# Kernel tuning notes

Hardware: AMD Instinct MI355X
Metric: run time of the kernel (lower is better)

The kernel has to match this reference:

```python
import jax, jax.numpy as jnp
import numpy as np

N_HEAD = 12

def setup_inputs() -> dict:
    key = jax.random.key(0)
    k1, k2, k3 = jax.random.split(key, 3)
    B, T, C = 8, 1024, 768
    x = jax.random.normal(k1, (B, T, C), dtype=jnp.float32)
    # torch nn.Linear weight layout: [out_features, in_features]
    W_attn = jax.random.normal(k2, (3 * C, C), dtype=jnp.float32) * 0.02
    b_attn = jax.random.normal(k3, (3 * C,), dtype=jnp.float32) * 0.02
    return {"x": x, "W_attn": W_attn, "b_attn": b_attn}

def reference(x, W_attn, b_attn):
    B, T, C = x.shape
    H = N_HEAD
    hs = C // H
    scale = 1.0 / jnp.sqrt(jnp.asarray(hs, x.dtype))
    # fused qkv projection: x @ W^T + b  -> [B, T, 3C]
    qkv = jnp.einsum('btc,oc->bto', x, W_attn) + b_attn
    qkv = qkv.reshape(B, T, 3, H, hs).transpose(2, 0, 3, 1, 4)  # [3, B, H, T, hs]
    q, k, v = qkv[0], qkv[1], qkv[2]
    scores = jnp.einsum('bhqd,bhkd->bhqk', q, k) * scale  # [B, H, T, T]
    causal = jnp.tril(jnp.ones((T, T), dtype=bool))
    # masked_fill(-inf) followed by ReLU == zero out masked positions after ReLU
    att = jnp.where(causal, jax.nn.relu(scores), jnp.zeros((), scores.dtype))
    y = jnp.einsum('bhqk,bhkd->bhqd', att, v)  # [B, H, T, hs]
    return y.transpose(0, 2, 1, 3).reshape(B, T, C)
```

## Files before the change

### kernel.cpp

```cpp
#include <hip/hip_runtime.h>
#include <hip/hip_bf16.h>
#include <stdint.h>

#define T_ 1024
#define C_ 768
#define H_ 12
#define HS 64

typedef __attribute__((ext_vector_type(8))) short bf16x8;
typedef __attribute__((ext_vector_type(4))) float f32x4;

#define GLOAD16(g, l) __builtin_amdgcn_global_load_lds( \
    (const __attribute__((address_space(1))) uint32_t*)(g), \
    (__attribute__((address_space(3))) uint32_t*)(l), 16, 0, 0)

__device__ __forceinline__ ushort f2b(float f) {
  uint32_t u = __builtin_bit_cast(uint32_t, f);
  u = (u + 0x7fffu + ((u >> 16) & 1u)) >> 16;
  return (ushort)u;
}

__global__ __launch_bounds__(256) void cvt_bf16(
    const float* __restrict__ x, const float* __restrict__ wt,
    ushort* __restrict__ xb, ushort* __restrict__ wb) {
  const int NX4 = 8192 * 768 / 4;
  const int NW4 = 2304 * 768 / 4;
  int i = blockIdx.x * 256 + threadIdx.x;
  int stride = gridDim.x * 256;
  for (int idx = i; idx < NX4; idx += stride) {
    float4 f = ((const float4*)x)[idx];
    ushort4 o;
    o.x = f2b(f.x); o.y = f2b(f.y); o.z = f2b(f.z); o.w = f2b(f.w);
    ((ushort4*)xb)[idx] = o;
  }
  for (int idx = i; idx < NW4; idx += stride) {
    float4 f = ((const float4*)wt)[idx];
    ushort4 o;
    o.x = f2b(f.x); o.y = f2b(f.y); o.z = f2b(f.z); o.w = f2b(f.w);
    ((ushort4*)wb)[idx] = o;
  }
}

__global__ __launch_bounds__(256) void qkv_gemm(
    const ushort* __restrict__ xb, const ushort* __restrict__ wb,
    const float* __restrict__ bias,
    ushort* __restrict__ qo, ushort* __restrict__ ko, ushort* __restrict__ vo) {
  __shared__ __align__(16) ushort As[128 * 64];
  __shared__ __align__(16) ushort Bs[128 * 64];
  const int tid = threadIdx.x, lane = tid & 63, w = tid >> 6;
  const int g = lane >> 4, l15 = lane & 15;
  const int m0 = blockIdx.y * 128, n0 = blockIdx.x * 128;
  const int wr = w >> 1, wc = w & 1;
  f32x4 acc[4][4] = {};

  for (int kk = 0; kk < 12; ++kk) {
    const int k0 = kk * 64;
    #pragma unroll
    for (int c = 0; c < 4; ++c) {
      int p = (w * 4 + c) * 64 + lane;
      int row = p >> 3, s = p & 7;
      int sc = (s ^ (row & 7)) * 8;
      GLOAD16(xb + (size_t)(m0 + row) * 768 + k0 + sc, (char*)As + (w * 4 + c) * 1024);
      GLOAD16(wb + (size_t)(n0 + row) * 768 + k0 + sc, (char*)Bs + (w * 4 + c) * 1024);
    }
    __syncthreads();
    #pragma unroll
    for (int kd = 0; kd < 2; ++kd) {
      bf16x8 af[4], bf[4];
      #pragma unroll
      for (int mi = 0; mi < 4; ++mi) {
        int row = wr * 64 + mi * 16 + l15;
        af[mi] = *(const bf16x8*)((const char*)As + row * 128 + (((kd * 4 + g) ^ (row & 7)) << 4));
      }
      #pragma unroll
      for (int ni = 0; ni < 4; ++ni) {
        int row = wc * 64 + ni * 16 + l15;
        bf[ni] = *(const bf16x8*)((const char*)Bs + row * 128 + (((kd * 4 + g) ^ (row & 7)) << 4));
      }
      #pragma unroll
      for (int mi = 0; mi < 4; ++mi)
        #pragma unroll
        for (int ni = 0; ni < 4; ++ni)
          acc[mi][ni] = __builtin_amdgcn_mfma_f32_16x16x32_bf16(af[mi], bf[ni], acc[mi][ni], 0, 0, 0);
    }
    __syncthreads();
  }

  const int which = n0 / 768;
  ushort* outp = (which == 0) ? qo : (which == 1) ? ko : vo;
  #pragma unroll
  for (int ni = 0; ni < 4; ++ni) {
    int n = n0 + wc * 64 + ni * 16 + l15;
    float bn = bias[n];
    int nin = n - which * 768;
    int h = nin >> 6, d = nin & 63;
    #pragma unroll
    for (int mi = 0; mi < 4; ++mi) {
      #pragma unroll
      for (int r = 0; r < 4; ++r) {
        int m = m0 + wr * 64 + mi * 16 + g * 4 + r;
        float val = acc[mi][ni][r] + bn;
        outp[((size_t)((m >> 10) * H_ + h) * T_ + (m & (T_ - 1))) * HS + d] = f2b(val);
      }
    }
  }
}

__global__ __launch_bounds__(256) void transpose_v(
    const ushort* __restrict__ v, ushort* __restrict__ vT) {
  __shared__ __align__(16) ushort Ts[64 * 64];
  const int tid = threadIdx.x;
  const int bh = blockIdx.x, tt = blockIdx.y;
  const size_t base = (size_t)bh * (T_ * HS);
  #pragma unroll
  for (int c = 0; c < 2; ++c) {
    int p = c * 256 + tid;
    int row = p >> 3, s = p & 7;
    *(uint4*)((char*)Ts + row * 128 + ((s ^ (row & 7)) << 4)) =
        *(const uint4*)(v + base + (size_t)(tt * 64 + row) * HS + s * 8);
  }
  __syncthreads();
  #pragma unroll
  for (int c = 0; c < 2; ++c) {
    int p = c * 256 + tid;
    int d = p >> 3, s = p & 7, t0 = s * 8;
    ushort tmp[8];
    #pragma unroll
    for (int j = 0; j < 8; ++j) {
      int t = t0 + j;
      tmp[j] = *(const ushort*)((const char*)Ts + t * 128 + ((2 * d) ^ ((t & 7) << 4)));
    }
    uint4 pk;
    pk.x = (uint)tmp[0] | ((uint)tmp[1] << 16);
    pk.y = (uint)tmp[2] | ((uint)tmp[3] << 16);
    pk.z = (uint)tmp[4] | ((uint)tmp[5] << 16);
    pk.w = (uint)tmp[6] | ((uint)tmp[7] << 16);
    *(uint4*)(vT + base + (size_t)d * T_ + tt * 64 + t0) = pk;
  }
}

__global__ __launch_bounds__(256) void attn_relu(
    const ushort* __restrict__ q, const ushort* __restrict__ k,
    const ushort* __restrict__ vT, float* __restrict__ out) {
  __shared__ __align__(16) ushort Qs[64 * 64];
  __shared__ __align__(16) ushort Ks[64 * 64];
  __shared__ __align__(16) ushort VTs[64 * 64];
  __shared__ __align__(16) ushort Ps[64 * 64];
  const int tid = threadIdx.x, lane = tid & 63, w = tid >> 6;
  const int g = lane >> 4, l15 = lane & 15;
  const int bh = blockIdx.x, qt = blockIdx.y;
  const int q0 = qt * 64;
  const size_t base = (size_t)bh * (T_ * HS);

  #pragma unroll
  for (int c = 0; c < 2; ++c) {
    int p = (w * 2 + c) * 64 + lane;
    int row = p >> 3, s = p & 7;
    int sc = (s ^ (row & 7)) * 8;
    GLOAD16(q + base + (size_t)(q0 + row) * HS + sc, (char*)Qs + (w * 2 + c) * 1024);
  }

  f32x4 yacc[4] = {};
  const int qrow = w * 16 + l15;
  const int nkt = qt + 1;

  for (int kt = 0; kt < nkt; ++kt) {
    #pragma unroll
    for (int c = 0; c < 2; ++c) {
      int p = (w * 2 + c) * 64 + lane;
      int row = p >> 3, s = p & 7;
      int sc = (s ^ (row & 7)) * 8;
      GLOAD16(k + base + (size_t)(kt * 64 + row) * HS + sc, (char*)Ks + (w * 2 + c) * 1024);
      GLOAD16(vT + base + (size_t)row * T_ + kt * 64 + sc, (char*)VTs + (w * 2 + c) * 1024);
    }
    __syncthreads();

    f32x4 sacc[4] = {};
    #pragma unroll
    for (int kd = 0; kd < 2; ++kd) {
      bf16x8 qf = *(const bf16x8*)((const char*)Qs + qrow * 128 + (((kd * 4 + g) ^ (qrow & 7)) << 4));
      #pragma unroll
      for (int nt = 0; nt < 4; ++nt) {
        int krow = nt * 16 + l15;
        bf16x8 kf = *(const bf16x8*)((const char*)Ks + krow * 128 + (((kd * 4 + g) ^ (krow & 7)) << 4));
        sacc[nt] = __builtin_amdgcn_mfma_f32_16x16x32_bf16(qf, kf, sacc[nt], 0, 0, 0);
      }
    }

    #pragma unroll
    for (int nt = 0; nt < 4; ++nt) {
      int kj = kt * 64 + nt * 16 + l15;
      #pragma unroll
      for (int r = 0; r < 4; ++r) {
        int i = w * 16 + g * 4 + r;
        float sv = sacc[nt][r] * 0.125f;
        float pv = (kj <= q0 + i) ? fmaxf(sv, 0.0f) : 0.0f;
        *(ushort*)((char*)Ps + i * 128 + (((nt * 16 + l15) * 2) ^ ((i & 7) << 4))) = f2b(pv);
      }
    }

    bf16x8 pf[2], vf[2][4];
    #pragma unroll
    for (int kj2 = 0; kj2 < 2; ++kj2) {
      pf[kj2] = *(const bf16x8*)((const char*)Ps + qrow * 128 + (((kj2 * 4 + g) ^ (qrow & 7)) << 4));
      #pragma unroll
      for (int nt = 0; nt < 4; ++nt) {
        int vrow = nt * 16 + l15;
        vf[kj2][nt] = *(const bf16x8*)((const char*)VTs + vrow * 128 + (((kj2 * 4 + g) ^ (vrow & 7)) << 4));
      }
    }
    #pragma unroll
    for (int kj2 = 0; kj2 < 2; ++kj2)
      #pragma unroll
      for (int nt = 0; nt < 4; ++nt)
        yacc[nt] = __builtin_amdgcn_mfma_f32_16x16x32_bf16(pf[kj2], vf[kj2][nt], yacc[nt], 0, 0, 0);

    __syncthreads();
  }

  const int bb = bh / H_, hh = bh % H_;
  #pragma unroll
  for (int nt = 0; nt < 4; ++nt) {
    #pragma unroll
    for (int r = 0; r < 4; ++r) {
      int t = q0 + w * 16 + g * 4 + r;
      int col = hh * HS + nt * 16 + l15;
      out[(size_t)(bb * T_ + t) * C_ + col] = yacc[nt][r];
    }
  }
}

extern "C" void kernel_launch(void* const* d_in, const int* in_sizes, int n_in,
                              void* d_out, int out_size, void* d_ws, size_t ws_size,
                              hipStream_t stream) {
  const float* x    = (const float*)d_in[0];
  const float* W    = (const float*)d_in[1];
  const float* bias = (const float*)d_in[2];
  float* out = (float*)d_out;

  char* ws = (char*)d_ws;
  ushort* xb = (ushort*)ws;
  ushort* wb = (ushort*)(ws + 12582912);
  ushort* qb = (ushort*)(ws + 16121856);
  ushort* kb = (ushort*)(ws + 28704768);
  ushort* vb = (ushort*)(ws + 41287680);
  ushort* vT = xb;

  cvt_bf16<<<2048, 256, 0, stream>>>(x, W, xb, wb);
  qkv_gemm<<<dim3(18, 64), 256, 0, stream>>>(xb, wb, bias, qb, kb, vb);
  transpose_v<<<dim3(96, 16), 256, 0, stream>>>(vb, vT);
  attn_relu<<<dim3(96, 16), 256, 0, stream>>>(qb, kb, vT, out);
}
```

Measured before the change: 174.5 us.

## Double-buffer GEMM and attention loads, fuse V transpose into QKV epilogue

The QKV GEMM now uses a double-buffered LDS pipeline over 32-wide K slices, prefetching the next slice while the current one is multiplied. Its V-output blocks write V transposed through shared memory, so the separate transpose kernel and one launch go away. The attention kernel double-buffers K/V tiles, keeps Q in registers, and reverses the query-tile order so the longest causal tiles are scheduled first. The costs are more LDS per block, which may lower occupancy, and a more complex epilogue.

```diff
diff --git a/kernel.cpp b/kernel.cpp
--- a/kernel.cpp
+++ b/kernel.cpp
@@ -44,146 +44,166 @@
 __global__ __launch_bounds__(256) void qkv_gemm(
     const ushort* __restrict__ xb, const ushort* __restrict__ wb,
     const float* __restrict__ bias,
-    ushort* __restrict__ qo, ushort* __restrict__ ko, ushort* __restrict__ vo) {
-  __shared__ __align__(16) ushort As[128 * 64];
-  __shared__ __align__(16) ushort Bs[128 * 64];
+    ushort* __restrict__ qo, ushort* __restrict__ ko, ushort* __restrict__ vT) {
+  __shared__ __align__(16) ushort smem[16384];
   const int tid = threadIdx.x, lane = tid & 63, w = tid >> 6;
   const int g = lane >> 4, l15 = lane & 15;
   const int m0 = blockIdx.y * 128, n0 = blockIdx.x * 128;
   const int wr = w >> 1, wc = w & 1;
   f32x4 acc[4][4] = {};
 
-  for (int kk = 0; kk < 12; ++kk) {
-    const int k0 = kk * 64;
-    #pragma unroll
-    for (int c = 0; c < 4; ++c) {
-      int p = (w * 4 + c) * 64 + lane;
-      int row = p >> 3, s = p & 7;
-      int sc = (s ^ (row & 7)) * 8;
-      GLOAD16(xb + (size_t)(m0 + row) * 768 + k0 + sc, (char*)As + (w * 4 + c) * 1024);
-      GLOAD16(wb + (size_t)(n0 + row) * 768 + k0 + sc, (char*)Bs + (w * 4 + c) * 1024);
-    }
+  const ushort* srcA[2];
+  const ushort* srcB[2];
+  int dstoff[2];
+  #pragma unroll
+  for (int c = 0; c < 2; ++c) {
+    int p = (c * 4 + w) * 64 + lane;
+    int row = p >> 2, s = p & 3;
+    int sc = (s ^ ((row >> 1) & 3)) * 8;
+    srcA[c] = xb + (size_t)(m0 + row) * 768 + sc;
+    srcB[c] = wb + (size_t)(n0 + row) * 768 + sc;
+    dstoff[c] = (c * 4 + w) * 1024;
+  }
+
+#define STAGE_G(buf, k0) do { \
+    char* bb_ = (char*)smem + (buf) * 16384; \
+    _Pragma("unroll") \
+    for (int c_ = 0; c_ < 2; ++c_) { \
+      GLOAD16(srcA[c_] + (k0), bb_ + dstoff[c_]); \
+      GLOAD16(srcB[c_] + (k0), bb_ + 8192 + dstoff[c_]); \
+    } \
+  } while (0)
+
+  int cur = 0;
+  STAGE_G(0, 0);
+  __syncthreads();
+  #pragma unroll 2
+  for (int kk = 0; kk < 24; ++kk) {
+    if (kk < 23) STAGE_G(cur ^ 1, (kk + 1) * 32);
+    const char* Ab = (const char*)smem + cur * 16384;
+    const char* Bb = Ab + 8192;
+    bf16x8 af[4], bfr[4];
+    #pragma unroll
+    for (int mi = 0; mi < 4; ++mi) {
+      int r = wr * 64 + mi * 16 + l15;
+      af[mi] = *(const bf16x8*)(Ab + r * 64 + ((g ^ ((r >> 1) & 3)) << 4));
+    }
+    #pragma unroll
+    for (int ni = 0; ni < 4; ++ni) {
+      int r = wc * 64 + ni * 16 + l15;
+      bfr[ni] = *(const bf16x8*)(Bb + r * 64 + ((g ^ ((r >> 1) & 3)) << 4));
+    }
+    #pragma unroll
+    for (int mi = 0; mi < 4; ++mi)
+      #pragma unroll
+      for (int ni = 0; ni < 4; ++ni)
+        acc[mi][ni] = __builtin_amdgcn_mfma_f32_16x16x32_bf16(af[mi], bfr[ni], acc[mi][ni], 0, 0, 0);
     __syncthreads();
-    #pragma unroll
-    for (int kd = 0; kd < 2; ++kd) {
-      bf16x8 af[4], bf[4];
+    cur ^= 1;
+  }
+
+  const int which = n0 / 768;
+  if (which < 2) {
+    ushort* outp = (which == 0) ? qo : ko;
+    #pragma unroll
+    for (int ni = 0; ni < 4; ++ni) {
+      int n = n0 + wc * 64 + ni * 16 + l15;
+      float bn = bias[n];
+      int nin = n - which * 768;
+      int h = nin >> 6, d = nin & 63;
       #pragma unroll
       for (int mi = 0; mi < 4; ++mi) {
-        int row = wr * 64 + mi * 16 + l15;
-        af[mi] = *(const bf16x8*)((const char*)As + row * 128 + (((kd * 4 + g) ^ (row & 7)) << 4));
-      }
-      #pragma unroll
-      for (int ni = 0; ni < 4; ++ni) {
-        int row = wc * 64 + ni * 16 + l15;
-        bf[ni] = *(const bf16x8*)((const char*)Bs + row * 128 + (((kd * 4 + g) ^ (row & 7)) << 4));
-      }
-      #pragma unroll
-      for (int mi = 0; mi < 4; ++mi)
         #pragma unroll
-        for (int ni = 0; ni < 4; ++ni)
-          acc[mi][ni] = __builtin_amdgcn_mfma_f32_16x16x32_bf16(af[mi], bf[ni], acc[mi][ni], 0, 0, 0);
+        for (int r = 0; r < 4; ++r) {
+          int m = m0 + wr * 64 + mi * 16 + g * 4 + r;
+          float val = acc[mi][ni][r] + bn;
+          outp[((size_t)((m >> 10) * H_ + h) * T_ + (m & (T_ - 1))) * HS + d] = f2b(val);
+        }
+      }
+    }
+  } else {
+    #pragma unroll
+    for (int ni = 0; ni < 4; ++ni) {
+      int n = n0 + wc * 64 + ni * 16 + l15;
+      float bn = bias[n];
+      int dl = wc * 64 + ni * 16 + l15;
+      #pragma unroll
+      for (int mi = 0; mi < 4; ++mi) {
+        #pragma unroll
+        for (int r = 0; r < 4; ++r) {
+          int tl = wr * 64 + mi * 16 + g * 4 + r;
+          *(ushort*)((char*)smem + dl * 256 + ((tl * 2) ^ ((dl & 7) << 4))) =
+              f2b(acc[mi][ni][r] + bn);
+        }
+      }
     }
     __syncthreads();
-  }
-
-  const int which = n0 / 768;
-  ushort* outp = (which == 0) ? qo : (which == 1) ? ko : vo;
-  #pragma unroll
-  for (int ni = 0; ni < 4; ++ni) {
-    int n = n0 + wc * 64 + ni * 16 + l15;
-    float bn = bias[n];
-    int nin = n - which * 768;
-    int h = nin >> 6, d = nin & 63;
-    #pragma unroll
-    for (int mi = 0; mi < 4; ++mi) {
-      #pragma unroll
-      for (int r = 0; r < 4; ++r) {
-        int m = m0 + wr * 64 + mi * 16 + g * 4 + r;
-        float val = acc[mi][ni][r] + bn;
-        outp[((size_t)((m >> 10) * H_ + h) * T_ + (m & (T_ - 1))) * HS + d] = f2b(val);
-      }
-    }
-  }
-}
-
-__global__ __launch_bounds__(256) void transpose_v(
-    const ushort* __restrict__ v, ushort* __restrict__ vT) {
-  __shared__ __align__(16) ushort Ts[64 * 64];
-  const int tid = threadIdx.x;
-  const int bh = blockIdx.x, tt = blockIdx.y;
-  const size_t base = (size_t)bh * (T_ * HS);
-  #pragma unroll
-  for (int c = 0; c < 2; ++c) {
-    int p = c * 256 + tid;
-    int row = p >> 3, s = p & 7;
-    *(uint4*)((char*)Ts + row * 128 + ((s ^ (row & 7)) << 4)) =
-        *(const uint4*)(v + base + (size_t)(tt * 64 + row) * HS + s * 8);
-  }
-  __syncthreads();
-  #pragma unroll
-  for (int c = 0; c < 2; ++c) {
-    int p = c * 256 + tid;
-    int d = p >> 3, s = p & 7, t0 = s * 8;
-    ushort tmp[8];
-    #pragma unroll
-    for (int j = 0; j < 8; ++j) {
-      int t = t0 + j;
-      tmp[j] = *(const ushort*)((const char*)Ts + t * 128 + ((2 * d) ^ ((t & 7) << 4)));
-    }
-    uint4 pk;
-    pk.x = (uint)tmp[0] | ((uint)tmp[1] << 16);
-    pk.y = (uint)tmp[2] | ((uint)tmp[3] << 16);
-    pk.z = (uint)tmp[4] | ((uint)tmp[5] << 16);
-    pk.w = (uint)tmp[6] | ((uint)tmp[7] << 16);
-    *(uint4*)(vT + base + (size_t)d * T_ + tt * 64 + t0) = pk;
+    const int b = m0 >> 10, t0base = m0 & 1023;
+    #pragma unroll
+    for (int c = 0; c < 8; ++c) {
+      int p = c * 256 + tid;
+      int dl = p >> 4, tch = p & 15;
+      uint4 val = *(const uint4*)((const char*)smem + dl * 256 + ((tch * 16) ^ ((dl & 7) << 4)));
+      int nin = n0 + dl - 1536;
+      int h = nin >> 6, dd = nin & 63;
+      *(uint4*)(vT + (((size_t)(b * H_ + h) * HS + dd) << 10) + t0base + tch * 8) = val;
+    }
   }
 }
 
 __global__ __launch_bounds__(256) void attn_relu(
     const ushort* __restrict__ q, const ushort* __restrict__ k,
     const ushort* __restrict__ vT, float* __restrict__ out) {
-  __shared__ __align__(16) ushort Qs[64 * 64];
-  __shared__ __align__(16) ushort Ks[64 * 64];
-  __shared__ __align__(16) ushort VTs[64 * 64];
-  __shared__ __align__(16) ushort Ps[64 * 64];
+  __shared__ __align__(16) ushort smem[20480];
   const int tid = threadIdx.x, lane = tid & 63, w = tid >> 6;
   const int g = lane >> 4, l15 = lane & 15;
-  const int bh = blockIdx.x, qt = blockIdx.y;
+  const int bh = blockIdx.x, qt = 15 - blockIdx.y;
   const int q0 = qt * 64;
   const size_t base = (size_t)bh * (T_ * HS);
-
+  const int qrow = w * 16 + l15;
+
+  bf16x8 qf[2];
+  #pragma unroll
+  for (int kd = 0; kd < 2; ++kd)
+    qf[kd] = *(const bf16x8*)(q + base + (size_t)(q0 + qrow) * HS + (kd * 4 + g) * 8);
+
+  int rowS[2], scS[2], dstoff[2];
   #pragma unroll
   for (int c = 0; c < 2; ++c) {
-    int p = (w * 2 + c) * 64 + lane;
-    int row = p >> 3, s = p & 7;
-    int sc = (s ^ (row & 7)) * 8;
-    GLOAD16(q + base + (size_t)(q0 + row) * HS + sc, (char*)Qs + (w * 2 + c) * 1024);
-  }
+    int p = (c * 4 + w) * 64 + lane;
+    rowS[c] = p >> 3;
+    scS[c] = ((p & 7) ^ (rowS[c] & 7)) * 8;
+    dstoff[c] = (c * 4 + w) * 1024;
+  }
+
+#define STAGE_KV(buf, kt) do { \
+    char* bb_ = (char*)smem + (buf) * 16384; \
+    _Pragma("unroll") \
+    for (int c_ = 0; c_ < 2; ++c_) { \
+      GLOAD16(k + base + (size_t)((kt) * 64 + rowS[c_]) * HS + scS[c_], bb_ + dstoff[c_]); \
+      GLOAD16(vT + base + (size_t)rowS[c_] * T_ + (kt) * 64 + scS[c_], bb_ + 8192 + dstoff[c_]); \
+    } \
+  } while (0)
 
   f32x4 yacc[4] = {};
-  const int qrow = w * 16 + l15;
   const int nkt = qt + 1;
-
+  int cur = 0;
+  STAGE_KV(0, 0);
+  __syncthreads();
   for (int kt = 0; kt < nkt; ++kt) {
-    #pragma unroll
-    for (int c = 0; c < 2; ++c) {
-      int p = (w * 2 + c) * 64 + lane;
-      int row = p >> 3, s = p & 7;
-      int sc = (s ^ (row & 7)) * 8;
-      GLOAD16(k + base + (size_t)(kt * 64 + row) * HS + sc, (char*)Ks + (w * 2 + c) * 1024);
-      GLOAD16(vT + base + (size_t)row * T_ + kt * 64 + sc, (char*)VTs + (w * 2 + c) * 1024);
-    }
-    __syncthreads();
+    if (kt + 1 < nkt) STAGE_KV(cur ^ 1, kt + 1);
+    const char* Kb = (const char*)smem + cur * 16384;
+    const char* Vb = Kb + 8192;
+    char* Pb = (char*)smem + 32768;
 
     f32x4 sacc[4] = {};
     #pragma unroll
     for (int kd = 0; kd < 2; ++kd) {
-      bf16x8 qf = *(const bf16x8*)((const char*)Qs + qrow * 128 + (((kd * 4 + g) ^ (qrow & 7)) << 4));
       #pragma unroll
       for (int nt = 0; nt < 4; ++nt) {
-        int krow = nt * 16 + l15;
-        bf16x8 kf = *(const bf16x8*)((const char*)Ks + krow * 128 + (((kd * 4 + g) ^ (krow & 7)) << 4));
-        sacc[nt] = __builtin_amdgcn_mfma_f32_16x16x32_bf16(qf, kf, sacc[nt], 0, 0, 0);
+        int kr = nt * 16 + l15;
+        bf16x8 kf = *(const bf16x8*)(Kb + kr * 128 + (((kd * 4 + g) ^ (kr & 7)) << 4));
+        sacc[nt] = __builtin_amdgcn_mfma_f32_16x16x32_bf16(qf[kd], kf, sacc[nt], 0, 0, 0);
       }
     }
 
@@ -195,18 +215,18 @@
         int i = w * 16 + g * 4 + r;
         float sv = sacc[nt][r] * 0.125f;
         float pv = (kj <= q0 + i) ? fmaxf(sv, 0.0f) : 0.0f;
-        *(ushort*)((char*)Ps + i * 128 + (((nt * 16 + l15) * 2) ^ ((i & 7) << 4))) = f2b(pv);
+        *(ushort*)(Pb + i * 128 + (((nt * 16 + l15) * 2) ^ ((i & 7) << 4))) = f2b(pv);
       }
     }
 
     bf16x8 pf[2], vf[2][4];
     #pragma unroll
     for (int kj2 = 0; kj2 < 2; ++kj2) {
-      pf[kj2] = *(const bf16x8*)((const char*)Ps + qrow * 128 + (((kj2 * 4 + g) ^ (qrow & 7)) << 4));
+      pf[kj2] = *(const bf16x8*)(Pb + qrow * 128 + (((kj2 * 4 + g) ^ (qrow & 7)) << 4));
       #pragma unroll
       for (int nt = 0; nt < 4; ++nt) {
-        int vrow = nt * 16 + l15;
-        vf[kj2][nt] = *(const bf16x8*)((const char*)VTs + vrow * 128 + (((kj2 * 4 + g) ^ (vrow & 7)) << 4));
+        int vr = nt * 16 + l15;
+        vf[kj2][nt] = *(const bf16x8*)(Vb + vr * 128 + (((kj2 * 4 + g) ^ (vr & 7)) << 4));
       }
     }
     #pragma unroll
@@ -216,6 +236,7 @@
         yacc[nt] = __builtin_amdgcn_mfma_f32_16x16x32_bf16(pf[kj2], vf[kj2][nt], yacc[nt], 0, 0, 0);
 
     __syncthreads();
+    cur ^= 1;
   }
 
   const int bb = bh / H_, hh = bh % H_;
@@ -243,11 +264,9 @@
   ushort* wb = (ushort*)(ws + 12582912);
   ushort* qb = (ushort*)(ws + 16121856);
   ushort* kb = (ushort*)(ws + 28704768);
-  ushort* vb = (ushort*)(ws + 41287680);
-  ushort* vT = xb;
+  ushort* vT = (ushort*)(ws + 41287680);
 
   cvt_bf16<<<2048, 256, 0, stream>>>(x, W, xb, wb);
-  qkv_gemm<<<dim3(18, 64), 256, 0, stream>>>(xb, wb, bias, qb, kb, vb);
-  transpose_v<<<dim3(96, 16), 256, 0, stream>>>(vb, vT);
+  qkv_gemm<<<dim3(18, 64), 256, 0, stream>>>(xb, wb, bias, qb, kb, vT);
   attn_relu<<<dim3(96, 16), 256, 0, stream>>>(qb, kb, vT, out);
 }
```

Measured after the change: 162.8 us. 1.07x faster.
